# Kernel tuning notes

Hardware: AMD Instinct MI355X
Metric: run time of the kernel (lower is better)

## Reference

```python
import jax, jax.numpy as jnp
import numpy as np

H = 16
D_MODEL = 1024
D_K = D_MODEL // H


def setup_inputs() -> dict:
    key = jax.random.key(0)
    kx, kq, kk, kv, ko = jax.random.split(key, 5)
    B, T = 4, 2048
    scale = 1.0 / np.sqrt(D_MODEL)
    return {
        "X": jax.random.normal(kx, (B, T, D_MODEL), dtype=jnp.float32),
        "W_q": jax.random.normal(kq, (D_MODEL, D_MODEL), dtype=jnp.float32) * scale,
        "W_k": jax.random.normal(kk, (D_MODEL, D_MODEL), dtype=jnp.float32) * scale,
        "W_v": jax.random.normal(kv, (D_MODEL, D_MODEL), dtype=jnp.float32) * scale,
        "W_o": jax.random.normal(ko, (D_MODEL, D_MODEL), dtype=jnp.float32) * scale,
    }


def reference(X, W_q, W_k, W_v, W_o):
    B, T, D = X.shape
    # projections (torch Linear: x @ W.T); weights stored as [out, in]=[D,D]
    Q = (X @ W_q.T).reshape(B, T, H, D_K).transpose(0, 2, 1, 3)  # [B,H,T,Dk]
    K = (X @ W_k.T).reshape(B, T, H, D_K).transpose(0, 2, 1, 3)
    V = (X @ W_v.T).reshape(B, T, H, D_K).transpose(0, 2, 1, 3)
    S = jnp.einsum("bhqd,bhkd->bhqk", Q, K) * (D_K ** -0.5)  # [B,H,T,T]
    causal = jnp.tril(jnp.ones((T, T), dtype=bool))
    S = jnp.where(causal, S, -jnp.inf)
    A = jax.nn.softmax(S, axis=-1)
    out = jnp.einsum("bhqk,bhkd->bhqd", A, V)  # [B,H,T,Dk]
    out = out.transpose(0, 2, 1, 3).reshape(B, T, D)
    return out @ W_o.T
```

## Files before the change

kernel.cpp:

```cpp
#include <hip/hip_runtime.h>
#include <hip/hip_bf16.h>

#define T_SEQ 2048
#define NB 4
#define NH 16
#define DK 64
#define DM 1024
#define QKS 2048

typedef __attribute__((ext_vector_type(8))) __bf16 bf16x8;
typedef __attribute__((ext_vector_type(4))) __bf16 bf16x4;
typedef __attribute__((ext_vector_type(4))) float f32x4;
typedef __attribute__((ext_vector_type(2))) int i32x2;
typedef __attribute__((ext_vector_type(4))) int i32x4;

__device__ __forceinline__ void gl_lds16(const __bf16* g, __bf16* l) {
  __builtin_amdgcn_global_load_lds(
      (const __attribute__((address_space(1))) void*)g,
      (__attribute__((address_space(3))) void*)l,
      16, 0, 0);
}

__device__ __forceinline__ unsigned cvt_pk_bf16(float lo, float hi) {
  unsigned r;
  asm("v_cvt_pk_bf16_f32 %0, %1, %2" : "=v"(r) : "v"(lo), "v"(hi));
  return r;
}

__global__ __launch_bounds__(256) void cast_all(const float* __restrict__ X,
                                                const float* __restrict__ Wq,
                                                const float* __restrict__ Wk,
                                                const float* __restrict__ Wv,
                                                const float* __restrict__ Wo,
                                                __bf16* __restrict__ Xb,
                                                __bf16* __restrict__ Wqb,
                                                __bf16* __restrict__ Wkb,
                                                __bf16* __restrict__ Wvb,
                                                __bf16* __restrict__ Wob) {
  const int NX4 = NB * T_SEQ * DM / 4;
  const int NW4 = DM * DM / 4;
  int i = blockIdx.x * 256 + threadIdx.x;
  const float* in;
  __bf16* out;
  int idx;
  if (i < NX4) {
    in = X; out = Xb; idx = i;
  } else {
    const int j = i - NX4;
    const int w = j >> 18;
    idx = j & (NW4 - 1);
    in = (w == 0) ? Wq : (w == 1) ? Wk : (w == 2) ? Wv : Wo;
    out = (w == 0) ? Wqb : (w == 1) ? Wkb : (w == 2) ? Wvb : Wob;
  }
  float4 v = reinterpret_cast<const float4*>(in)[idx];
  bf16x4 o;
  o[0] = (__bf16)v.x; o[1] = (__bf16)v.y; o[2] = (__bf16)v.z; o[3] = (__bf16)v.w;
  reinterpret_cast<bf16x4*>(out)[idx] = o;
}

template<int DO_QSCALE>
__global__ __launch_bounds__(512, 2) void gemm_nt_8p(const __bf16* __restrict__ A,
                                                     const __bf16* __restrict__ Bm,
                                                     __bf16* __restrict__ C,
                                                     int M, int N, int K) {
  __shared__ alignas(16) __bf16 As[2][256][64];
  __shared__ alignas(16) __bf16 Bs[2][256][64];
  const int tid = threadIdx.x;
  const int wid = tid >> 6, l = tid & 63, lg = l >> 4, lr = l & 15;
  const int wm = wid >> 2, wn = wid & 3;
  const int f = (int)blockIdx.x;
  const int cpx = (int)gridDim.x >> 3;
  const int swz = (f & 7) * cpx + (f >> 3);
  const int nbn = N >> 8;
  const int m0 = (swz / nbn) << 8, n0 = (swz % nbn) << 8;

  const int srow = l >> 3;
  const int schunk = (l & 7) ^ srow;
  const int rsw = lr & 7;
  const int strow = wid * 8 + srow;

  f32x4 acc[8][4] = {};
  bf16x8 aA[8], bB[8];

  auto SA = [&](int buf, int half, int t) {
    #pragma unroll
    for (int j = 0; j < 2; ++j)
      gl_lds16(A + (size_t)(m0 + half * 128 + j * 64 + strow) * K + t * 64 + schunk * 8,
               &As[buf][half * 128 + j * 64 + wid * 8][0]);
  };
  auto SB = [&](int buf, int half, int t) {
    #pragma unroll
    for (int j = 0; j < 2; ++j)
      gl_lds16(Bm + (size_t)(n0 + half * 128 + j * 64 + strow) * K + t * 64 + schunk * 8,
               &Bs[buf][half * 128 + j * 64 + wid * 8][0]);
  };
  auto LA = [&](int buf, int mh) {
    #pragma unroll
    for (int mt = 0; mt < 4; ++mt) {
      const char* p = (const char*)&As[buf][wm * 128 + mh * 64 + mt * 16 + lr][0];
      aA[mt * 2 + 0] = *reinterpret_cast<const bf16x8*>(p + ((lg ^ rsw) << 4));
      aA[mt * 2 + 1] = *reinterpret_cast<const bf16x8*>(p + (((4 + lg) ^ rsw) << 4));
    }
  };
  auto LBh = [&](int buf, int nh) {
    #pragma unroll
    for (int ntl = 0; ntl < 2; ++ntl) {
      const int nt = nh * 2 + ntl;
      const char* p = (const char*)&Bs[buf][wn * 64 + nt * 16 + lr][0];
      bB[nt * 2 + 0] = *reinterpret_cast<const bf16x8*>(p + ((lg ^ rsw) << 4));
      bB[nt * 2 + 1] = *reinterpret_cast<const bf16x8*>(p + (((4 + lg) ^ rsw) << 4));
    }
  };
  auto MQ = [&](int mh, int nh) {
    #pragma unroll
    for (int mt = 0; mt < 4; ++mt)
      #pragma unroll
      for (int ntl = 0; ntl < 2; ++ntl) {
        const int nt = nh * 2 + ntl;
        acc[mh * 4 + mt][nt] = __builtin_amdgcn_mfma_f32_16x16x32_bf16(
            aA[mt * 2 + 0], bB[nt * 2 + 0], acc[mh * 4 + mt][nt], 0, 0, 0);
        acc[mh * 4 + mt][nt] = __builtin_amdgcn_mfma_f32_16x16x32_bf16(
            aA[mt * 2 + 1], bB[nt * 2 + 1], acc[mh * 4 + mt][nt], 0, 0, 0);
      }
  };
  #define WAIT_LGKM() do { asm volatile("s_waitcnt lgkmcnt(0)" ::: "memory"); \
                           __builtin_amdgcn_sched_barrier(0); } while (0)

  SB(0, 0, 0); SB(0, 1, 0); SA(0, 0, 0); SA(0, 1, 0);
  SB(1, 0, 1); SB(1, 1, 1); SA(1, 0, 1);
  asm volatile("s_waitcnt vmcnt(6)" ::: "memory");
  __builtin_amdgcn_s_barrier();

  const int NIT = K >> 7;
  for (int i = 0; i < NIT; ++i) {
    const bool lastit = (i == NIT - 1);
    const int t2 = 2 * i + 2, t3 = 2 * i + 3;
    LA(0, 0); LBh(0, 0);
    SA(1, 1, 2 * i + 1);
    __builtin_amdgcn_s_barrier();
    WAIT_LGKM();
    __builtin_amdgcn_s_setprio(1); MQ(0, 0); __builtin_amdgcn_s_setprio(0);
    __builtin_amdgcn_s_barrier();
    LBh(0, 1);
    WAIT_LGKM();
    __builtin_amdgcn_s_setprio(1); MQ(0, 1); __builtin_amdgcn_s_setprio(0);
    __builtin_amdgcn_s_barrier();
    LA(0, 1);
    if (!lastit) { SB(0, 0, t2); SB(0, 1, t2); }
    __builtin_amdgcn_s_barrier();
    WAIT_LGKM();
    __builtin_amdgcn_s_setprio(1); MQ(1, 1); __builtin_amdgcn_s_setprio(0);
    __builtin_amdgcn_s_barrier();
    if (!lastit) SA(0, 0, t2);
    __builtin_amdgcn_s_setprio(1); MQ(1, 0); __builtin_amdgcn_s_setprio(0);
    if (lastit) asm volatile("s_waitcnt vmcnt(0)" ::: "memory");
    else        asm volatile("s_waitcnt vmcnt(6)" ::: "memory");
    __builtin_amdgcn_s_barrier();
    LA(1, 0); LBh(1, 0);
    if (!lastit) SA(0, 1, t2);
    __builtin_amdgcn_s_barrier();
    WAIT_LGKM();
    __builtin_amdgcn_s_setprio(1); MQ(0, 0); __builtin_amdgcn_s_setprio(0);
    __builtin_amdgcn_s_barrier();
    LBh(1, 1);
    WAIT_LGKM();
    __builtin_amdgcn_s_setprio(1); MQ(0, 1); __builtin_amdgcn_s_setprio(0);
    __builtin_amdgcn_s_barrier();
    LA(1, 1);
    if (!lastit) { SB(1, 0, t3); SB(1, 1, t3); }
    __builtin_amdgcn_s_barrier();
    WAIT_LGKM();
    __builtin_amdgcn_s_setprio(1); MQ(1, 1); __builtin_amdgcn_s_setprio(0);
    __builtin_amdgcn_s_barrier();
    if (!lastit) SA(1, 0, t3);
    __builtin_amdgcn_s_setprio(1); MQ(1, 0); __builtin_amdgcn_s_setprio(0);
    if (!lastit) asm volatile("s_waitcnt vmcnt(6)" ::: "memory");
    __builtin_amdgcn_s_barrier();
  }

  #pragma unroll
  for (int mt = 0; mt < 8; ++mt)
    #pragma unroll
    for (int nt = 0; nt < 4; ++nt) {
      const int ng = n0 + wn * 64 + nt * 16 + lr;
      const float sc = (DO_QSCALE && ng < 1024) ? 0.18033688f : 1.0f;
      #pragma unroll
      for (int r = 0; r < 4; ++r) {
        const int mg = m0 + wm * 128 + mt * 16 + 4 * lg + r;
        C[(size_t)mg * N + ng] = (__bf16)(acc[mt][nt][r] * sc);
      }
    }
  #undef WAIT_LGKM
}

template<typename CT, int MODE>
__global__ __launch_bounds__(256, 2) void gemm_nt(const __bf16* __restrict__ A,
                                                  const __bf16* __restrict__ B,
                                                  CT* __restrict__ C,
                                                  int M, int N, int K) {
  __shared__ alignas(16) __bf16 As[128][64];
  __shared__ alignas(16) __bf16 Bs[128][64];
  const int tid = threadIdx.x;
  const int m0 = blockIdx.y * 128, n0 = blockIdx.x * 128;
  const int w = tid >> 6, l = tid & 63, lg = l >> 4, lr = l & 15;
  const int wr = (w >> 1) * 64, wc = (w & 1) * 64;
  const int srow = l >> 3;
  const int schunk = (l & 7) ^ srow;

  f32x4 acc[4][4] = {};
  const int rsw = lr & 7;

  for (int k0 = 0; k0 < K; k0 += 64) {
    __syncthreads();
    #pragma unroll
    for (int j = 0; j < 4; ++j) {
      const int rbase = (w * 4 + j) * 8;
      gl_lds16(A + (size_t)(m0 + rbase + srow) * K + k0 + schunk * 8, &As[rbase][0]);
      gl_lds16(B + (size_t)(n0 + rbase + srow) * K + k0 + schunk * 8, &Bs[rbase][0]);
    }
    asm volatile("s_waitcnt vmcnt(0)" ::: "memory");
    __syncthreads();
    #pragma unroll
    for (int kk = 0; kk < 2; ++kk) {
      bf16x8 af[4], bfr[4];
      #pragma unroll
      for (int mt = 0; mt < 4; ++mt) {
        const char* p = (const char*)&As[wr + mt * 16 + lr][0];
        af[mt] = *reinterpret_cast<const bf16x8*>(p + (((kk * 4 + lg) ^ rsw) << 4));
      }
      #pragma unroll
      for (int nt = 0; nt < 4; ++nt) {
        const char* p = (const char*)&Bs[wc + nt * 16 + lr][0];
        bfr[nt] = *reinterpret_cast<const bf16x8*>(p + (((kk * 4 + lg) ^ rsw) << 4));
      }
      __builtin_amdgcn_s_setprio(1);
      #pragma unroll
      for (int mt = 0; mt < 4; ++mt)
        #pragma unroll
        for (int nt = 0; nt < 4; ++nt)
          acc[mt][nt] = __builtin_amdgcn_mfma_f32_16x16x32_bf16(af[mt], bfr[nt], acc[mt][nt], 0, 0, 0);
      __builtin_amdgcn_s_setprio(0);
    }
  }
  #pragma unroll
  for (int mt = 0; mt < 4; ++mt)
    #pragma unroll
    for (int nt = 0; nt < 4; ++nt)
      #pragma unroll
      for (int r = 0; r < 4; ++r) {
        const int mg = m0 + wr + mt * 16 + 4 * lg + r;
        int ng = n0 + wc + nt * 16 + lr;
        if (MODE == 2)
          ng = (ng & ~31) | (8 * (lr >> 2) + (lr & 3) + ((nt & 1) << 2));
        C[(size_t)mg * N + ng] = (CT)acc[mt][nt][r];
      }
}

__global__ __launch_bounds__(256, 2) void attn_fwd(const __bf16* __restrict__ QK,
                                                   const __bf16* __restrict__ VT,
                                                   __bf16* __restrict__ AO) {
  __shared__ alignas(16) __bf16 Ks[2][2][64][64];
  __shared__ alignas(16) __bf16 Vs[2][2][64][64];
  const int tid = threadIdx.x;
  const int w = tid >> 6, l = tid & 63, lg = l >> 4, lr = l & 15;

  const int fl = (int)blockIdx.x + 8 * (int)blockIdx.y;
  const int bh = ((fl & 7) << 3) | ((fl >> 3) & 7);
  const int c = fl >> 6;
  const int b = bh >> 4, h = bh & 15;
  const size_t bT = (size_t)b * T_SEQ;
  const int M = NB * T_SEQ;

  const int srow = l >> 3;
  const int schunk = (l & 7) ^ srow;
  const __bf16* Kg = QK + bT * QKS + 1024 + h * DK;
  const __bf16* Vg = VT + (size_t)(h * DK) * M + bT;
  const int rsw = lr & 7;

  bf16x8 vone;
  #pragma unroll
  for (int j = 0; j < 8; ++j) vone[j] = (__bf16)1.0f;

  const int qbA = c, qbB = 15 - c, qbC = 16 + c, qbD = 31 - c;
  const int qrwA = qbA * 64 + w * 16, qrwB = qbB * 64 + w * 16;
  const int qrwC = qbC * 64 + w * 16, qrwD = qbD * 64 + w * 16;
  const int klA = qbA * 64, klB = qbB * 64, klC = qbC * 64, klD = qbD * 64;

  const __bf16* QpA = QK + (bT + qrwA + lr) * QKS + h * DK;
  const __bf16* QpB = QK + (bT + qrwB + lr) * QKS + h * DK;
  const __bf16* QpC = QK + (bT + qrwC + lr) * QKS + h * DK;
  const __bf16* QpD = QK + (bT + qrwD + lr) * QKS + h * DK;
  const bf16x8 qfA0 = *reinterpret_cast<const bf16x8*>(QpA + 8 * lg);
  const bf16x8 qfA1 = *reinterpret_cast<const bf16x8*>(QpA + 32 + 8 * lg);
  const bf16x8 qfB0 = *reinterpret_cast<const bf16x8*>(QpB + 8 * lg);
  const bf16x8 qfB1 = *reinterpret_cast<const bf16x8*>(QpB + 32 + 8 * lg);
  const bf16x8 qfC0 = *reinterpret_cast<const bf16x8*>(QpC + 8 * lg);
  const bf16x8 qfC1 = *reinterpret_cast<const bf16x8*>(QpC + 32 + 8 * lg);
  const bf16x8 qfD0 = *reinterpret_cast<const bf16x8*>(QpD + 8 * lg);
  const bf16x8 qfD1 = *reinterpret_cast<const bf16x8*>(QpD + 32 + 8 * lg);

  f32x4 o_accA[4] = {}, o_accB[4] = {}, o_accC[4] = {}, o_accD[4] = {};
  f32x4 lA = {}, lB = {}, lC = {}, lD = {};

  auto STAGE = [&](int buf, int st, int kbase) {
    #pragma unroll
    for (int i = 0; i < 2; ++i) {
      const int seg = w * 2 + i;
      gl_lds16(Kg + (size_t)(kbase + seg * 8 + srow) * QKS + schunk * 8,
               &Ks[buf][st][seg * 8][0]);
      gl_lds16(Vg + (size_t)(seg * 8 + srow) * M + kbase + schunk * 8,
               &Vs[buf][st][seg * 8][0]);
    }
  };

  auto CHUNK = [&](const bf16x8& qf0, const bf16x8& qf1, f32x4* o_acc,
                   f32x4& l_acc, int qrw, bool masked, int k0,
                   const bf16x8* kf, const bf16x8* vf) {
    f32x4 s[4] = {};
    __builtin_amdgcn_s_setprio(1);
    #pragma unroll
    for (int ct = 0; ct < 4; ++ct) {
      s[ct] = __builtin_amdgcn_mfma_f32_16x16x32_bf16(kf[2 * ct], qf0, s[ct], 0, 0, 0);
      s[ct] = __builtin_amdgcn_mfma_f32_16x16x32_bf16(kf[2 * ct + 1], qf1, s[ct], 0, 0, 0);
    }
    __builtin_amdgcn_s_setprio(0);
    if (masked) {
      #pragma unroll
      for (int ct = 0; ct < 4; ++ct)
        #pragma unroll
        for (int r = 0; r < 4; ++r)
          if (k0 + 16 * ct + 4 * lg + r > qrw + lr) s[ct][r] = -1e30f;
    }
    unsigned pk[4][2];
    #pragma unroll
    for (int ct = 0; ct < 4; ++ct) {
      const float p0 = __builtin_amdgcn_exp2f(s[ct][0]);
      const float p1 = __builtin_amdgcn_exp2f(s[ct][1]);
      const float p2 = __builtin_amdgcn_exp2f(s[ct][2]);
      const float p3 = __builtin_amdgcn_exp2f(s[ct][3]);
      pk[ct][0] = cvt_pk_bf16(p0, p1);
      pk[ct][1] = cvt_pk_bf16(p2, p3);
    }
    const bf16x8 pf0 = __builtin_bit_cast(bf16x8, i32x4{(int)pk[0][0], (int)pk[0][1],
                                                        (int)pk[1][0], (int)pk[1][1]});
    const bf16x8 pf1 = __builtin_bit_cast(bf16x8, i32x4{(int)pk[2][0], (int)pk[2][1],
                                                        (int)pk[3][0], (int)pk[3][1]});
    __builtin_amdgcn_s_setprio(1);
    l_acc = __builtin_amdgcn_mfma_f32_16x16x32_bf16(pf0, vone, l_acc, 0, 0, 0);
    l_acc = __builtin_amdgcn_mfma_f32_16x16x32_bf16(pf1, vone, l_acc, 0, 0, 0);
    #pragma unroll
    for (int dt = 0; dt < 4; ++dt) {
      o_acc[dt] = __builtin_amdgcn_mfma_f32_16x16x32_bf16(pf0, vf[2 * dt],     o_acc[dt], 0, 0, 0);
      o_acc[dt] = __builtin_amdgcn_mfma_f32_16x16x32_bf16(pf1, vf[2 * dt + 1], o_acc[dt], 0, 0, 0);
    }
    __builtin_amdgcn_s_setprio(0);
  };

  STAGE(0, 0, 0);
  STAGE(0, 1, 64);
  asm volatile("s_waitcnt vmcnt(0)" ::: "memory");
  __syncthreads();
  int buf = 0;

  for (int k0 = 0; k0 <= klD; k0 += 128) {
    if (k0 + 128 <= klD) STAGE(buf ^ 1, 0, k0 + 128);
    if (k0 + 192 <= klD) STAGE(buf ^ 1, 1, k0 + 192);

    #pragma unroll
    for (int st = 0; st < 2; ++st) {
      const int kk = k0 + st * 64;
      if (kk > klD) break;
      bf16x8 kf[8], vf[8];
      #pragma unroll
      for (int ct = 0; ct < 4; ++ct) {
        const char* kb = (const char*)&Ks[buf][st][ct * 16 + lr][0];
        kf[2 * ct]     = *reinterpret_cast<const bf16x8*>(kb + ((lg ^ rsw) << 4));
        kf[2 * ct + 1] = *reinterpret_cast<const bf16x8*>(kb + (((lg + 4) ^ rsw) << 4));
        const char* vb = (const char*)&Vs[buf][st][ct * 16 + lr][0];
        vf[2 * ct]     = *reinterpret_cast<const bf16x8*>(vb + ((lg ^ rsw) << 4));
        vf[2 * ct + 1] = *reinterpret_cast<const bf16x8*>(vb + (((lg + 4) ^ rsw) << 4));
      }
      CHUNK(qfD0, qfD1, o_accD, lD, qrwD, kk == klD, kk, kf, vf);
      if (kk <= klC) CHUNK(qfC0, qfC1, o_accC, lC, qrwC, kk == klC, kk, kf, vf);
      if (kk <= klB) CHUNK(qfB0, qfB1, o_accB, lB, qrwB, kk == klB, kk, kf, vf);
      if (kk <= klA) CHUNK(qfA0, qfA1, o_accA, lA, qrwA, kk == klA, kk, kf, vf);
    }

    asm volatile("s_waitcnt vmcnt(0)" ::: "memory");
    __syncthreads();
    buf ^= 1;
  }

  #pragma unroll
  for (int cc = 0; cc < 4; ++cc) {
    const f32x4& la = (cc == 0) ? lA : (cc == 1) ? lB : (cc == 2) ? lC : lD;
    f32x4* oa = (cc == 0) ? o_accA : (cc == 1) ? o_accB : (cc == 2) ? o_accC : o_accD;
    const int qrw = (cc == 0) ? qrwA : (cc == 1) ? qrwB : (cc == 2) ? qrwC : qrwD;
    #pragma unroll
    for (int r = 0; r < 4; ++r) {
      const float inv = 1.0f / la[r];
      #pragma unroll
      for (int dt = 0; dt < 4; ++dt) {
        const int rg = qrw + 4 * lg + r;
        const int cg = h * DK + dt * 16 + lr;
        AO[(bT + rg) * DM + cg] = (__bf16)(oa[dt][r] * inv);
      }
    }
  }
}

extern "C" void kernel_launch(void* const* d_in, const int* in_sizes, int n_in,
                              void* d_out, int out_size, void* d_ws, size_t ws_size,
                              hipStream_t stream) {
  (void)in_sizes; (void)n_in; (void)out_size; (void)ws_size;
  const float* X  = (const float*)d_in[0];
  const float* Wq = (const float*)d_in[1];
  const float* Wk = (const float*)d_in[2];
  const float* Wv = (const float*)d_in[3];
  const float* Wo = (const float*)d_in[4];
  float* OUT = (float*)d_out;

  char* ws = (char*)d_ws;
  const size_t SZ_X  = (size_t)NB * T_SEQ * DM * 2;
  const size_t SZ_W  = (size_t)DM * DM * 2;
  const size_t SZ_QK = (size_t)NB * T_SEQ * QKS * 2;
  __bf16* Xb  = (__bf16*)ws; ws += SZ_X;
  __bf16* Wqb = (__bf16*)ws; ws += SZ_W;
  __bf16* Wkb = (__bf16*)ws; ws += SZ_W;
  __bf16* Wvb = (__bf16*)ws; ws += SZ_W;
  __bf16* Wob = (__bf16*)ws; ws += SZ_W;
  __bf16* QKb = (__bf16*)ws; ws += SZ_QK;
  __bf16* VTb = (__bf16*)ws; ws += SZ_X;
  __bf16* AOb = (__bf16*)ws; ws += SZ_X;

  const int M = NB * T_SEQ;

  cast_all<<<(M * DM / 4 + 4 * DM * DM / 4) / 256, 256, 0, stream>>>(
      X, Wq, Wk, Wv, Wo, Xb, Wqb, Wkb, Wvb, Wob);

  gemm_nt_8p<1><<<(M / 256) * (QKS / 256), 512, 0, stream>>>(Xb, Wqb, QKb, M, QKS, DM);
  gemm_nt<__bf16, 2><<<dim3(M / 128, DM / 128), 256, 0, stream>>>(Wvb, Xb, VTb, DM, M, DM);
  attn_fwd<<<dim3(8, NB * NH), 256, 0, stream>>>(QKb, VTb, AOb);
  gemm_nt<float, 0><<<dim3(DM / 128, M / 128), 256, 0, stream>>>(AOb, Wob, OUT, M, DM, DM);
}
```

Before: 142.2 us.

## Fuse V projection into QK GEMM and add separate V transpose kernel

Widens the fused projection GEMM from Q|K to Q|K|V by treating the contiguous Wq, Wk, Wv buffers as one 3072-row weight, and drops the separate transposed V GEMM. A new small kernel transposes the V slice through LDS into the permuted V^T layout that attention expects. AO now reuses the X buffer. This removes one GEMM launch and its second pass over X, in exchange for an extra write and read of V plus a transpose kernel with strided scalar LDS reads.

```diff
diff --git a/kernel.cpp b/kernel.cpp
--- a/kernel.cpp
+++ b/kernel.cpp
@@ -6,7 +6,7 @@
 #define NH 16
 #define DK 64
 #define DM 1024
-#define QKS 2048
+#define QKS 3072
 
 typedef __attribute__((ext_vector_type(8))) __bf16 bf16x8;
 typedef __attribute__((ext_vector_type(4))) __bf16 bf16x4;
@@ -193,7 +193,41 @@
   #undef WAIT_LGKM
 }
 
-template<typename CT, int MODE>
+__global__ __launch_bounds__(256) void vtrans_sigma(const __bf16* __restrict__ QKV,
+                                                    __bf16* __restrict__ VT) {
+  __shared__ alignas(16) __bf16 T[64][80];
+  const int t = threadIdx.x;
+  const int kt = (int)blockIdx.x;
+  const int bh = (int)blockIdx.y;
+  const int b = bh >> 4, h = bh & 15;
+  const size_t bT = (size_t)b * T_SEQ;
+  const int M = NB * T_SEQ;
+  {
+    const int r = t >> 2, cch = t & 3;
+    const __bf16* src = QKV + (bT + kt * 64 + r) * QKS + 2048 + h * DK + cch * 16;
+    const bf16x8 v0 = *reinterpret_cast<const bf16x8*>(src);
+    const bf16x8 v1 = *reinterpret_cast<const bf16x8*>(src + 8);
+    *reinterpret_cast<bf16x8*>(&T[r][cch * 16]) = v0;
+    *reinterpret_cast<bf16x8*>(&T[r][cch * 16 + 8]) = v1;
+  }
+  __syncthreads();
+  const int d = t >> 2, kc = t & 3;
+  __bf16* dst = VT + (size_t)(h * DK + d) * M + bT + kt * 64 + kc * 16;
+  #pragma unroll
+  for (int g = 0; g < 2; ++g) {
+    bf16x8 o;
+    #pragma unroll
+    for (int j = 0; j < 8; ++j) {
+      const int s = kc * 16 + g * 8 + j;
+      const int s5 = s & 31;
+      const int ks = (s & 32) | (s5 & 3) | (((s5 >> 2) & 1) << 4) | (((s5 >> 3) & 3) << 2);
+      o[j] = T[ks][d];
+    }
+    *reinterpret_cast<bf16x8*>(dst + g * 8) = o;
+  }
+}
+
+template<typename CT>
 __global__ __launch_bounds__(256, 2) void gemm_nt(const __bf16* __restrict__ A,
                                                   const __bf16* __restrict__ B,
                                                   CT* __restrict__ C,
@@ -249,9 +283,7 @@
       #pragma unroll
       for (int r = 0; r < 4; ++r) {
         const int mg = m0 + wr + mt * 16 + 4 * lg + r;
-        int ng = n0 + wc + nt * 16 + lr;
-        if (MODE == 2)
-          ng = (ng & ~31) | (8 * (lr >> 2) + (lr & 3) + ((nt & 1) << 2));
+        const int ng = n0 + wc + nt * 16 + lr;
         C[(size_t)mg * N + ng] = (CT)acc[mt][nt][r];
       }
 }
@@ -421,25 +453,25 @@
   float* OUT = (float*)d_out;
 
   char* ws = (char*)d_ws;
-  const size_t SZ_X  = (size_t)NB * T_SEQ * DM * 2;
-  const size_t SZ_W  = (size_t)DM * DM * 2;
-  const size_t SZ_QK = (size_t)NB * T_SEQ * QKS * 2;
-  __bf16* Xb  = (__bf16*)ws; ws += SZ_X;
-  __bf16* Wqb = (__bf16*)ws; ws += SZ_W;
-  __bf16* Wkb = (__bf16*)ws; ws += SZ_W;
-  __bf16* Wvb = (__bf16*)ws; ws += SZ_W;
-  __bf16* Wob = (__bf16*)ws; ws += SZ_W;
-  __bf16* QKb = (__bf16*)ws; ws += SZ_QK;
-  __bf16* VTb = (__bf16*)ws; ws += SZ_X;
-  __bf16* AOb = (__bf16*)ws; ws += SZ_X;
+  const size_t SZ_X   = (size_t)NB * T_SEQ * DM * 2;
+  const size_t SZ_W   = (size_t)DM * DM * 2;
+  const size_t SZ_QKV = (size_t)NB * T_SEQ * QKS * 2;
+  __bf16* Xb   = (__bf16*)ws; ws += SZ_X;
+  __bf16* Wqb  = (__bf16*)ws; ws += SZ_W;
+  __bf16* Wkb  = (__bf16*)ws; ws += SZ_W;
+  __bf16* Wvb  = (__bf16*)ws; ws += SZ_W;
+  __bf16* Wob  = (__bf16*)ws; ws += SZ_W;
+  __bf16* QKVb = (__bf16*)ws; ws += SZ_QKV;
+  __bf16* VTb  = (__bf16*)ws; ws += SZ_X;
+  __bf16* AOb  = Xb;
 
   const int M = NB * T_SEQ;
 
   cast_all<<<(M * DM / 4 + 4 * DM * DM / 4) / 256, 256, 0, stream>>>(
       X, Wq, Wk, Wv, Wo, Xb, Wqb, Wkb, Wvb, Wob);
 
-  gemm_nt_8p<1><<<(M / 256) * (QKS / 256), 512, 0, stream>>>(Xb, Wqb, QKb, M, QKS, DM);
-  gemm_nt<__bf16, 2><<<dim3(M / 128, DM / 128), 256, 0, stream>>>(Wvb, Xb, VTb, DM, M, DM);
-  attn_fwd<<<dim3(8, NB * NH), 256, 0, stream>>>(QKb, VTb, AOb);
-  gemm_nt<float, 0><<<dim3(DM / 128, M / 128), 256, 0, stream>>>(AOb, Wob, OUT, M, DM, DM);
-}
+  gemm_nt_8p<1><<<(M / 256) * (QKS / 256), 512, 0, stream>>>(Xb, Wqb, QKVb, M, QKS, DM);
+  vtrans_sigma<<<dim3(T_SEQ / 64, NB * NH), 256, 0, stream>>>(QKVb, VTb);
+  attn_fwd<<<dim3(8, NB * NH), 256, 0, stream>>>(QKVb, VTb, AOb);
+  gemm_nt<float><<<dim3(DM / 128, M / 128), 256, 0, stream>>>(AOb, Wob, OUT, M, DM, DM);
+}
```

Measured after the change: 161.7 us. +13.8%, slower.
